# Kernel optimization log

Hardware: AMD Instinct MI355X
Metric: run time of the kernel (lower is better)

## Reference

```python
import jax, jax.numpy as jnp
import numpy as np


def _filters(bmt):
    # bmt: (L,) low-pass h(-m1..m2). dec_lo = flip(h); g_tilde = flip(h)*(-1)^j;
    # dec_hi = flip(g_tilde)  (matches bmt_h / bmt_g_tilde / bmt_g in the torch code)
    L = bmt.shape[0]
    signs = 1.0 - 2.0 * (jnp.arange(L) % 2).astype(bmt.dtype)  # (+1,-1,+1,...)
    dec_lo = jnp.flip(bmt)
    g_tilde = dec_lo * signs
    dec_hi = jnp.flip(g_tilde)
    return dec_lo, dec_hi


def _conv_stride2(xp, w):
    # xp: (B,1,Npad), w: (L,) -> cross-correlation, stride 2, valid (== torch conv1d)
    return jax.lax.conv_general_dilated(xp, w[None, None, :], window_strides=(2,), padding='VALID')


def _dwt(x, dec_lo, dec_hi, m1, m2):
    # x: (B,K,N) -> (a, d) each (B,K,N//2). Periodic padding:
    # pad_periodic(x,n1,n2)[i] = x[(i-n1) mod N]  ==  jnp.pad mode='wrap'.
    B, K, N = x.shape
    xr = x.reshape(B * K, 1, N)
    xa = jnp.pad(xr, ((0, 0), (0, 0), (m1, m2)), mode='wrap')
    a = _conv_stride2(xa, dec_lo)
    xd = jnp.pad(xr, ((0, 0), (0, 0), (m2 - 1, m1 + 1)), mode='wrap')
    d = _conv_stride2(xd, dec_hi)
    return a.reshape(B, K, N // 2), d.reshape(B, K, N // 2)


def setup_inputs() -> dict:
    key = jax.random.key(0)
    k1, k2 = jax.random.split(key)
    x = jax.random.normal(k1, (32, 1024, 1024), dtype=jnp.float32)
    bmt = jax.random.normal(k2, (8,), dtype=jnp.float32)
    return {"x": x, "bmt": bmt, "m1": 3, "m2": 4}


def reference(x, bmt, m1, m2):
    # 2D fast wavelet transform in square format (Wav_2d_sqformat)
    dec_lo, dec_hi = _filters(bmt)
    cA, cD = _dwt(x, dec_lo, dec_hi, m1, m2)                       # rows filtered
    cAA, cAD = _dwt(cA.swapaxes(1, 2), dec_lo, dec_hi, m1, m2)     # cols of cA
    cDA, cDD = _dwt(cD.swapaxes(1, 2), dec_lo, dec_hi, m1, m2)     # cols of cD
    cAA, cAD = cAA.swapaxes(1, 2), cAD.swapaxes(1, 2)
    cDA, cDD = cDA.swapaxes(1, 2), cDD.swapaxes(1, 2)
    top = jnp.concatenate([cAA, cAD], axis=2)
    bot = jnp.concatenate([cDA, cDD], axis=2)
    return jnp.concatenate([top, bot], axis=1)  # (B,N,N)
```

## Files before the change

### kernel.cpp

```cpp
#include <hip/hip_runtime.h>

#define NN 1024
#define HH 512
#define TR 32
#define TC 32
#define PR (2*TR+8)
#define PC (2*TC+8)

__global__ __launch_bounds__(256) void dwt2d_fused(const float* __restrict__ x,
                                                   const float* __restrict__ bmt,
                                                   float* __restrict__ out) {
    __shared__ float Xs[PR][PC + 1];
    __shared__ float A1s[PR][TC + 1];
    __shared__ float D1s[PR][TC + 1];

    const int tid = threadIdx.x;
    const int b  = blockIdx.z;
    const int R0 = blockIdx.y * TR;
    const int C0 = blockIdx.x * TC;

    float lo[8], hi[8];
#pragma unroll
    for (int j = 0; j < 8; ++j) lo[j] = bmt[7 - j];
#pragma unroll
    for (int j = 0; j < 8; ++j) { float v = bmt[j]; hi[j] = (j & 1) ? v : -v; }

    const float* xb = x + (size_t)b * NN * NN;

    const int rbase = 2 * R0 - 3;
    const int cbase = 2 * C0 - 3;
    for (int idx = tid; idx < PR * PC; idx += 256) {
        int u = idx / PC;
        int v = idx - u * PC;
        int rr = (rbase + u) & (NN - 1);
        int cc = (cbase + v) & (NN - 1);
        Xs[u][v] = xb[rr * NN + cc];
    }
    __syncthreads();

    for (int pos = tid; pos < PR * TC; pos += 256) {
        int u = pos >> 5;
        int c = pos & 31;
        float a = 0.f, d = 0.f;
#pragma unroll
        for (int j = 0; j < 8; ++j) {
            float v = Xs[u][2 * c + j];
            a += lo[j] * v;
            d += hi[j] * v;
        }
        A1s[u][c] = a;
        D1s[u][c] = d;
    }
    __syncthreads();

    const int c  = tid & 31;
    const int r0 = tid >> 5;
    float* ob = out + (size_t)b * NN * NN;
#pragma unroll
    for (int k = 0; k < TR / 8; ++k) {
        int r = r0 + k * 8;
        float aa = 0.f, ad = 0.f, da = 0.f, dd = 0.f;
#pragma unroll
        for (int j = 0; j < 8; ++j) {
            float a1 = A1s[2 * r + j][c];
            float d1 = D1s[2 * r + j][c];
            aa += lo[j] * a1;
            ad += hi[j] * a1;
            da += lo[j] * d1;
            dd += hi[j] * d1;
        }
        int orow = R0 + r;
        int ocol = C0 + c;
        ob[(size_t)orow * NN + ocol]            = aa;
        ob[(size_t)orow * NN + ocol + HH]       = ad;
        ob[(size_t)(orow + HH) * NN + ocol]      = da;
        ob[(size_t)(orow + HH) * NN + ocol + HH] = dd;
    }
}

extern "C" void kernel_launch(void* const* d_in, const int* in_sizes, int n_in,
                              void* d_out, int out_size, void* d_ws, size_t ws_size,
                              hipStream_t stream) {
    const float* x   = (const float*)d_in[0];
    const float* bmt = (const float*)d_in[1];
    float* out = (float*)d_out;
    const int B = in_sizes[0] / (NN * NN);
    dim3 grid(HH / TC, HH / TR, B);
    dwt2d_fused<<<grid, 256, 0, stream>>>(x, bmt, out);
}
```

Baseline: 255.5 us.

## Load input rows with float4 directly into registers and drop the input LDS tile

Removes the shared-memory staging of the raw input tile. Each thread instead loads 16 contiguous floats per row with float4 vector reads, or wrapped scalar reads at the periodic borders, and computes four row-filter outputs in registers before writing them to shared memory. This cuts LDS traffic and one barrier, and the smaller shared footprint together with launch_bounds(256,8) aims for higher occupancy. In exchange each thread uses more registers and overlapping windows are loaded redundantly from global memory/cache.

```diff
diff --git a/kernel.cpp b/kernel.cpp
--- a/kernel.cpp
+++ b/kernel.cpp
@@ -4,15 +4,14 @@
 #define HH 512
 #define TR 32
 #define TC 32
-#define PR (2*TR+8)
-#define PC (2*TC+8)
+#define S1R 72
+#define LST 33
 
-__global__ __launch_bounds__(256) void dwt2d_fused(const float* __restrict__ x,
-                                                   const float* __restrict__ bmt,
-                                                   float* __restrict__ out) {
-    __shared__ float Xs[PR][PC + 1];
-    __shared__ float A1s[PR][TC + 1];
-    __shared__ float D1s[PR][TC + 1];
+__global__ __launch_bounds__(256, 8) void dwt2d_fused(const float* __restrict__ x,
+                                                      const float* __restrict__ bmt,
+                                                      float* __restrict__ out) {
+    __shared__ float A1s[S1R][LST];
+    __shared__ float D1s[S1R][LST];
 
     const int tid = threadIdx.x;
     const int b  = blockIdx.z;
@@ -26,30 +25,40 @@
     for (int j = 0; j < 8; ++j) { float v = bmt[j]; hi[j] = (j & 1) ? v : -v; }
 
     const float* xb = x + (size_t)b * NN * NN;
+    const int rbase = 2 * R0 - 3;
+    const int gcol0 = 2 * C0 - 4;
+    const bool interior = (gcol0 >= 0) && (gcol0 + 72 <= NN);
 
-    const int rbase = 2 * R0 - 3;
-    const int cbase = 2 * C0 - 3;
-    for (int idx = tid; idx < PR * PC; idx += 256) {
-        int u = idx / PC;
-        int v = idx - u * PC;
-        int rr = (rbase + u) & (NN - 1);
-        int cc = (cbase + v) & (NN - 1);
-        Xs[u][v] = xb[rr * NN + cc];
-    }
-    __syncthreads();
-
-    for (int pos = tid; pos < PR * TC; pos += 256) {
-        int u = pos >> 5;
-        int c = pos & 31;
-        float a = 0.f, d = 0.f;
+    for (int idx = tid; idx < S1R * 8; idx += 256) {
+        int u  = idx >> 3;
+        int cg = idx & 7;
+        int row = (rbase + u) & (NN - 1);
+        const float* xr = xb + (size_t)row * NN;
+        int gb = gcol0 + 8 * cg;
+        float p[16];
+        if (interior) {
+            const float4* xv = (const float4*)(xr + gb);
 #pragma unroll
-        for (int j = 0; j < 8; ++j) {
-            float v = Xs[u][2 * c + j];
-            a += lo[j] * v;
-            d += hi[j] * v;
+            for (int q = 0; q < 4; ++q) {
+                float4 v = xv[q];
+                p[4*q+0] = v.x; p[4*q+1] = v.y; p[4*q+2] = v.z; p[4*q+3] = v.w;
+            }
+        } else {
+#pragma unroll
+            for (int t = 0; t < 16; ++t) p[t] = xr[(gb + t) & (NN - 1)];
         }
-        A1s[u][c] = a;
-        D1s[u][c] = d;
+#pragma unroll
+        for (int i = 0; i < 4; ++i) {
+            float a = 0.f, d = 0.f;
+#pragma unroll
+            for (int j = 0; j < 8; ++j) {
+                float v = p[2*i + 1 + j];
+                a += lo[j] * v;
+                d += hi[j] * v;
+            }
+            A1s[u][4*cg + i] = a;
+            D1s[u][4*cg + i] = d;
+        }
     }
     __syncthreads();
 
@@ -71,8 +80,8 @@
         }
         int orow = R0 + r;
         int ocol = C0 + c;
-        ob[(size_t)orow * NN + ocol]            = aa;
-        ob[(size_t)orow * NN + ocol + HH]       = ad;
+        ob[(size_t)orow * NN + ocol]             = aa;
+        ob[(size_t)orow * NN + ocol + HH]        = ad;
         ob[(size_t)(orow + HH) * NN + ocol]      = da;
         ob[(size_t)(orow + HH) * NN + ocol + HH] = dd;
     }
```

Result: slower. 273.5 us (+7.0%).
